# Kernel optimization log

Hardware: AMD Instinct MI355X
Metric: run time of the kernel (lower is better)

Reference implementation:

```python
import math
import jax, jax.numpy as jnp
import numpy as np

N_HEAD = 16
N_EMBD = 1024
HEAD_DIM = N_EMBD // N_HEAD  # 64
SHARED = 16
PRIV = HEAD_DIM - SHARED     # 48
B, T = 4, 2048
STD = 0.02


def setup_inputs() -> dict:
    key = jax.random.key(0)
    ks = jax.random.split(key, 6)
    x = jax.random.normal(ks[0], (B, T, N_EMBD), dtype=jnp.float32)
    # Linear params stored as (in, out); bias zeros per _reset_parameters
    W_share = jax.random.normal(ks[1], (N_EMBD, SHARED), dtype=jnp.float32) * STD
    Wq = jax.random.normal(ks[2], (N_EMBD, N_HEAD * PRIV), dtype=jnp.float32) * STD
    Wk = jax.random.normal(ks[3], (N_EMBD, N_HEAD * PRIV), dtype=jnp.float32) * STD
    Wv = jax.random.normal(ks[4], (N_EMBD, N_EMBD), dtype=jnp.float32) * STD
    Wo = jax.random.normal(ks[5], (N_EMBD, N_EMBD), dtype=jnp.float32) * STD
    return {
        'hidden_states': x,
        'W_share': W_share, 'b_share': jnp.zeros((SHARED,), jnp.float32),
        'Wq': Wq, 'bq': jnp.zeros((N_HEAD * PRIV,), jnp.float32),
        'Wk': Wk, 'bk': jnp.zeros((N_HEAD * PRIV,), jnp.float32),
        'Wv': Wv, 'bv': jnp.zeros((N_EMBD,), jnp.float32),
        'Wo': Wo, 'bo': jnp.zeros((N_EMBD,), jnp.float32),
    }


def reference(hidden_states, W_share, b_share, Wq, bq, Wk, bk, Wv, bv, Wo, bo):
    x = hidden_states
    Bt, Tt, C = x.shape
    # shared projection, broadcast across heads: (B,T,s) -> (B,H,T,s)
    share = x @ W_share + b_share
    share_h = jnp.broadcast_to(share[:, None, :, :], (Bt, N_HEAD, Tt, SHARED))
    # private q/k: (B,T,H*p) -> (B,H,T,p)
    q_priv = (x @ Wq + bq).reshape(Bt, Tt, N_HEAD, PRIV).transpose(0, 2, 1, 3)
    k_priv = (x @ Wk + bk).reshape(Bt, Tt, N_HEAD, PRIV).transpose(0, 2, 1, 3)
    q = jnp.concatenate([share_h, q_priv], axis=-1)  # (B,H,T,head_dim)
    k = jnp.concatenate([share_h, k_priv], axis=-1)
    v = (x @ Wv + bv).reshape(Bt, Tt, N_HEAD, HEAD_DIM).transpose(0, 2, 1, 3)
    scale = 1.0 / math.sqrt(HEAD_DIM)
    att = jnp.einsum('bhqd,bhkd->bhqk', q, k) * scale
    causal = jnp.tril(jnp.ones((Tt, Tt), dtype=bool))
    att = jnp.where(causal[None, None, :, :], att, -jnp.inf)
    att = jax.nn.softmax(att, axis=-1)
    y = jnp.einsum('bhqk,bhkd->bhqd', att, v)
    y = y.transpose(0, 2, 1, 3).reshape(Bt, Tt, C)
    y = y @ Wo + bo
    return y
```

## Files before the change

### kernel.cpp

```cpp
#include <hip/hip_runtime.h>
#include <hip/hip_bf16.h>

typedef unsigned short u16;
typedef short short8 __attribute__((ext_vector_type(8)));
typedef float f32x4 __attribute__((ext_vector_type(4)));
typedef float f32x16 __attribute__((ext_vector_type(16)));
typedef unsigned uint32x4 __attribute__((ext_vector_type(4)));

#define N_EMBD   1024
#define N_HEADS  16
#define HEAD_DIM 64
#define PRIV     48
#define SEQ_T    2048
#define BATCH    4
#define M_ROWS   (BATCH*SEQ_T)
#define PNS      2816
#define NTILES   (SEQ_T/64)
#define NT_K     16

#if __has_builtin(__builtin_amdgcn_exp2f)
#define EXP2(x) __builtin_amdgcn_exp2f(x)
#else
#define EXP2(x) exp2f(x)
#endif

#if __has_builtin(__builtin_amdgcn_global_load_lds)
#define HAVE_GLL 1
#else
#define HAVE_GLL 0
#endif

#if __has_builtin(__builtin_amdgcn_permlane32_swap)
#define HAVE_PLSWAP 1
typedef unsigned uint2v __attribute__((ext_vector_type(2)));
#else
#define HAVE_PLSWAP 0
#endif

__device__ __forceinline__ u16 f2bf(float f) {
  __hip_bfloat16 h = __float2bfloat16(f);
  return *reinterpret_cast<u16*>(&h);
}
__device__ __forceinline__ float bf2f(u16 s) {
  __hip_bfloat16 h;
  *reinterpret_cast<u16*>(&h) = s;
  return __bfloat162float(h);
}
__device__ __forceinline__ float loadv(const void* p, size_t i, int isf32) {
  return isf32 ? ((const float*)p)[i] : bf2f(((const u16*)p)[i]);
}
__device__ __forceinline__ u16 truncbf(float f) {
  unsigned u = __builtin_bit_cast(unsigned, f);
  return (u16)(u >> 16);
}
#if HAVE_GLL
__device__ __forceinline__ void gload_lds16(const u16* g, u16* l) {
  __builtin_amdgcn_global_load_lds(
      (const __attribute__((address_space(1))) void*)g,
      (__attribute__((address_space(3))) void*)l, 16, 0, 0);
}
#endif

__global__ __launch_bounds__(256) void detect_kernel(const u16* __restrict__ x,
                                                     int* __restrict__ flag) {
  __shared__ int cnt;
  if (threadIdx.x == 0) cnt = 0;
  __syncthreads();
  u16 v = x[2 * threadIdx.x];
  int e = (v >> 7) & 0xFF;
  int junk = (e >= 0xC0 || (e != 0 && e <= 0x30)) ? 1 : 0;
  if (junk) atomicAdd(&cnt, 1);
  __syncthreads();
  if (threadIdx.x == 0) *flag = (cnt > 16) ? 1 : 0;
}

__global__ __launch_bounds__(256) void pack_t_kernel(
    const void* __restrict__ Wsh, const void* __restrict__ Wq,
    const void* __restrict__ Wk,  const void* __restrict__ Wv,
    const void* __restrict__ Wo,
    const void* __restrict__ bsh, const void* __restrict__ bq,
    const void* __restrict__ bk,  const void* __restrict__ bv,
    const void* __restrict__ bo,
    u16* __restrict__ Wcat, u16* __restrict__ Woc,
    u16* __restrict__ bcat, u16* __restrict__ boc,
    const int* __restrict__ flagp)
{
  const int f = *flagp;
  if (blockIdx.z == 5) {
    const int flat = blockIdx.y * 16 + blockIdx.x;
    const int padN = (PNS - 2576) * 1024;
    for (int i = flat * 256 + threadIdx.x; i < padN; i += 256 * 256)
      Wcat[(size_t)2576 * 1024 + i] = 0;
    if (flat == 0) {
      for (int c = threadIdx.x; c < PNS; c += 256) {
        float v = 0.f;
        if (c < 16)        v = loadv(bsh, c, f);
        else if (c < 784)  v = loadv(bq, c - 16, f);
        else if (c < 1552) v = loadv(bk, c - 784, f);
        else if (c < 2576) v = loadv(bv, c - 1552, f);
        bcat[c] = f2bf(v);
      }
    } else if (flat == 1) {
      for (int c = threadIdx.x; c < N_EMBD; c += 256)
        boc[c] = f2bf(loadv(bo, c, f));
    }
    return;
  }
  const void* src; u16* dst; int N, rowOff;
  switch (blockIdx.z) {
    case 0: src = Wsh; dst = Wcat; N = 16;   rowOff = 0;    break;
    case 1: src = Wq;  dst = Wcat; N = 768;  rowOff = 16;   break;
    case 2: src = Wk;  dst = Wcat; N = 768;  rowOff = 784;  break;
    case 3: src = Wv;  dst = Wcat; N = 1024; rowOff = 1552; break;
    default:src = Wo;  dst = Woc;  N = 1024; rowOff = 0;    break;
  }
  const int n0 = blockIdx.x * 64;
  if (n0 >= N) return;
  const int k0 = blockIdx.y * 64;
  __shared__ u16 t[64][65];
  const int tx = threadIdx.x & 63, ty = threadIdx.x >> 6;
#pragma unroll
  for (int rr = 0; rr < 16; rr++) {
    int k = k0 + ty * 16 + rr;
    int n = n0 + tx;
    float v = (n < N) ? loadv(src, (size_t)k * N + n, f) : 0.f;
    t[ty * 16 + rr][tx] = f2bf(v);
  }
  __syncthreads();
#pragma unroll
  for (int rr = 0; rr < 16; rr++) {
    int n = ty * 16 + rr;
    if (n0 + n < N)
      dst[(size_t)(rowOff + n0 + n) * 1024 + k0 + tx] = t[tx][n];
  }
}

__global__ __launch_bounds__(256) void xbf_kernel(const void* __restrict__ x,
                                                  u16* __restrict__ Xb,
                                                  const int* __restrict__ flagp) {
  const int f = *flagp;
  const size_t i = (size_t)blockIdx.x * 256 + threadIdx.x;
  if (f) {
    const float4* p = (const float4*)x;
    float4 a = p[i * 2], b = p[i * 2 + 1];
    u16 t[8] = {f2bf(a.x), f2bf(a.y), f2bf(a.z), f2bf(a.w),
                f2bf(b.x), f2bf(b.y), f2bf(b.z), f2bf(b.w)};
    *(uint4*)&Xb[i * 8] = *(const uint4*)t;
  } else {
    *(uint4*)&Xb[i * 8] = ((const uint4*)x)[i];
  }
}

__global__ __launch_bounds__(512, 2) void gemm8p_kernel(
    const u16* __restrict__ A,
    const u16* __restrict__ Bt,
    const u16* __restrict__ bias,
    void* __restrict__ C, int ldc, int Mtiles,
    const int* __restrict__ flagp, int c_dyn)
{
  __shared__ __align__(16) u16 smem[73728];
  u16* const As = smem;
  u16* const Bs = smem + 3 * 8192;

  const bool cf32 = (c_dyn != 0) && (*flagp != 0);

  const int tid  = threadIdx.x;
  const int lane = tid & 63;
  const int w    = tid >> 6;
  const int quad = lane >> 4, l16 = lane & 15;
  const int wm   = w >> 2, wn = w & 3;

  const int nwg = gridDim.x;
  const int wg  = (blockIdx.x & 7) * (nwg >> 3) + (blockIdx.x >> 3);
  const int mb  = wg % Mtiles, nb = wg / Mtiles;
  const int m0  = mb * 128, n0 = nb * 256;

  int ldsA[2]; size_t glA[2];
  int ldsB[2][2]; size_t glB[2][2];
#pragma unroll
  for (int rd = 0; rd < 2; rd++) {
    int j = tid + rd * 512, rp = j >> 3, s = j & 7;
    int cl = (s ^ (rp & 7)) * 8;
    ldsA[rd] = rp * 64 + s * 8;
    glA[rd]  = (size_t)(m0 + rp) * 1024 + cl;
#pragma unroll
    for (int nh = 0; nh < 2; nh++) {
      int cc = (rp & 31) + nh * 32 + (rp >> 5) * 64;
      ldsB[nh][rd] = cc * 64 + s * 8;
      glB[nh][rd]  = (size_t)(n0 + cc) * 1024 + cl;
    }
  }

#if HAVE_GLL
#define G8(g, l) gload_lds16((g), (l))
#else
#define G8(g, l) (*(uint4*)(l) = *(const uint4*)(g))
#endif
#define STG_A(t, bf)                                                       \
  if ((t) < NT_K) {                                                        \
    _Pragma("unroll") for (int rd = 0; rd < 2; rd++)                       \
      G8(A + glA[rd] + (t) * 64, As + (bf) * 8192 + ldsA[rd]);             \
  }
#define STG_B(nh, t, bf)                                                   \
  if ((t) < NT_K) {                                                        \
    _Pragma("unroll") for (int rd = 0; rd < 2; rd++)                       \
      G8(Bt + glB[nh][rd] + (t) * 64, Bs + (bf) * 16384 + ldsB[nh][rd]);   \
  }

  const int ck0  = ((quad)     ^ (l16 & 7)) * 8;
  const int ck1  = ((4 + quad) ^ (l16 & 7)) * 8;
  const int arow = (wm * 64 + l16) * 64;
  const int brow = (wn * 64 + l16) * 64;

  f32x4 acc[4][4];
#pragma unroll
  for (int i = 0; i < 4; i++)
#pragma unroll
    for (int j = 0; j < 4; j++) acc[i][j] = (f32x4){0.f, 0.f, 0.f, 0.f};

  short8 af[4][2], bA[2][2], bB[2][2];

#define READ_A(cur)                                                        \
  { const u16* pa = As + (cur) * 8192 + arow;                              \
    _Pragma("unroll") for (int m = 0; m < 4; m++) {                        \
      af[m][0] = *(const short8*)(pa + m * 1024 + ck0);                    \
      af[m][1] = *(const short8*)(pa + m * 1024 + ck1); } }
#define READ_B(dst, nh, cur)                                               \
  { const u16* pb = Bs + (cur) * 16384 + brow + (nh) * 2048;               \
    _Pragma("unroll") for (int n = 0; n < 2; n++) {                        \
      dst[n][0] = *(const short8*)(pb + n * 1024 + ck0);                   \
      dst[n][1] = *(const short8*)(pb + n * 1024 + ck1); } }
#define MM16(bfr, nh)                                                      \
  __builtin_amdgcn_s_setprio(1);                                           \
  _Pragma("unroll") for (int m = 0; m < 4; m++)                            \
    _Pragma("unroll") for (int n = 0; n < 2; n++) {                        \
      acc[m][(nh)*2+n] = __builtin_amdgcn_mfma_f32_16x16x32_bf16(          \
          af[m][0], bfr[n][0], acc[m][(nh)*2+n], 0, 0, 0);                 \
      acc[m][(nh)*2+n] = __builtin_amdgcn_mfma_f32_16x16x32_bf16(          \
          af[m][1], bfr[n][1], acc[m][(nh)*2+n], 0, 0, 0); }               \
  __builtin_amdgcn_s_setprio(0);
#define BARR { __builtin_amdgcn_s_barrier(); __builtin_amdgcn_sched_barrier(0); }

  STG_A(0, 0); STG_B(1, 0, 0); STG_B(0, 0, 0);
  STG_A(1, 1); STG_B(1, 1, 1); STG_B(0, 1, 1);
  asm volatile("s_waitcnt vmcnt(6)");
  BARR;

#pragma unroll
  for (int kt = 0; kt < NT_K; kt++) {
    const int cur = kt % 3;
    const int stb = (kt + 2) % 3;
    READ_A(cur); READ_B(bA, 0, cur);
    STG_A(kt + 2, stb); STG_B(1, kt + 2, stb);
    BARR;
    MM16(bA, 0);
    BARR;
    READ_B(bB, 1, cur);
    STG_B(0, kt + 2, stb);
    BARR;
    MM16(bB, 1);
    if (kt < NT_K - 2)       { asm volatile("s_waitcnt vmcnt(6)"); }
    else if (kt == NT_K - 2) { asm volatile("s_waitcnt vmcnt(0)"); }
    BARR;
  }
#undef STG_A
#undef STG_B
#undef READ_A
#undef READ_B
#undef MM16
#undef BARR
#undef G8

  float bvv[4];
#pragma unroll
  for (int ni = 0; ni < 4; ni++)
    bvv[ni] = bf2f(bias[n0 + wn * 64 + ni * 16 + l16]);

  if (!cf32) {
    u16* cs = smem + w * 4096;
#pragma unroll
    for (int m = 0; m < 4; m++)
#pragma unroll
      for (int ni = 0; ni < 4; ni++)
#pragma unroll
        for (int r = 0; r < 4; r++) {
          int row = m * 16 + quad * 4 + r;
          int ch  = ((ni * 2 + (l16 >> 3)) ^ (row & 7)) * 8 + (l16 & 7);
          cs[row * 64 + ch] = f2bf(acc[m][ni][r] + bvv[ni]);
        }
    u16* Cb = (u16*)C;
#pragma unroll
    for (int i = 0; i < 8; i++) {
      int ch = lane + i * 64;
      int rr = ch >> 3, cc = ch & 7;
      short8 v = *(const short8*)(cs + rr * 64 + ((cc ^ (rr & 7)) * 8));
      *(short8*)&Cb[(size_t)(m0 + wm * 64 + rr) * ldc + n0 + wn * 64 + cc * 8] = v;
    }
  } else {
    float* cf = (float*)(void*)smem + w * 2048;
#pragma unroll
    for (int pass = 0; pass < 2; pass++) {
#pragma unroll
      for (int m2 = 0; m2 < 2; m2++)
#pragma unroll
        for (int ni = 0; ni < 4; ni++)
#pragma unroll
          for (int r = 0; r < 4; r++) {
            int row = m2 * 16 + quad * 4 + r;
            int ch  = ((ni * 4 + (l16 >> 2)) ^ (row & 15)) * 4 + (l16 & 3);
            cf[row * 64 + ch] = acc[pass * 2 + m2][ni][r] + bvv[ni];
          }
      float* Cf = (float*)C;
#pragma unroll
      for (int i = 0; i < 8; i++) {
        int ch = lane + i * 64;
        int rr = ch >> 4, cc = ch & 15;
        f32x4 v = *(const f32x4*)(cf + rr * 64 + ((cc ^ (rr & 15)) * 4));
        *(f32x4*)&Cf[(size_t)(m0 + wm * 64 + pass * 32 + rr) * ldc +
                     n0 + wn * 64 + cc * 4] = v;
      }
    }
  }
}

__global__ __launch_bounds__(256) void vt_kernel(const u16* __restrict__ P,
                                                 u16* __restrict__ Vt)
{
  const int tt = blockIdx.x * 64;
  const int bh = blockIdx.y;
  const int b = bh >> 4, h = bh & 15;
  const int vcol = 1552 + h * HEAD_DIM;
  __shared__ u16 t[64][65];
  const int tx = threadIdx.x & 63, ty = threadIdx.x >> 6;
#pragma unroll
  for (int rr = 0; rr < 16; rr++) {
    int r = ty * 16 + rr;
    t[r][tx] = P[((size_t)b * SEQ_T + tt + r) * PNS + vcol + tx];
  }
  __syncthreads();
#pragma unroll
  for (int rr = 0; rr < 16; rr++) {
    int d = ty * 16 + rr;
    Vt[((size_t)bh * 64 + d) * SEQ_T + tt + tx] = t[tx][d];
  }
}

__global__ __launch_bounds__(256, 3) void attn_kernel(
    const u16* __restrict__ P, const u16* __restrict__ Vt,
    u16* __restrict__ Y)
{
  const int bh  = blockIdx.x;
  const int b   = bh >> 4, h = bh & 15;
  const int j   = blockIdx.y;
  const int qtA = 2 * j, qtB = 2 * j + 1;
  const int tid = threadIdx.x;
  const int w   = tid >> 6;
  const int lane = tid & 63;
  const int l32 = lane & 31, hi = lane >> 5;
  const size_t rowb = (size_t)b * SEQ_T;
  const int qcol = 16 + h * PRIV;
  const int kcol = 784 + h * PRIV;

  __shared__ __align__(16) u16 Ks[3][64 * 64];
  __shared__ __align__(16) u16 Vs[3][64 * 64];

  const float csc = 0.18033688011112042f;
  const int iA = qtA * 64 + w * 16, iB = qtB * 64 + w * 16;
  const int gi = (l32 < 16) ? (iA + l32) : (iB + l32 - 16);
  const u16* qptr = P + (rowb + gi) * PNS;

  short8 qb[4];
  qb[0] = *(const short8*)&qptr[8 * hi];
#pragma unroll
  for (int c = 1; c < 4; c++)
    qb[c] = *(const short8*)&qptr[qcol + 16 * c + 8 * hi - 16];
#pragma unroll
  for (int c = 0; c < 4; c++)
#pragma unroll
    for (int e = 0; e < 8; e++)
      qb[c][e] = (short)f2bf(bf2f((u16)qb[c][e]) * csc);

  short8 ones;
#pragma unroll
  for (int e = 0; e < 8; e++) ones[e] = (short)0x3F80;

  const int nkt = qtB + 1;

#if HAVE_GLL
#define GLOADA(g, l) gload_lds16((g), (l))
#else
#define GLOADA(g, l) (*(uint4*)(l) = *(const uint4*)(g))
#endif
#define STAGE_KV(t, bb)                                                        \
  {                                                                            \
    const int kk0 = (t) * 64;                                                  \
    _Pragma("unroll") for (int i2 = 0; i2 < 2; i2++) {                         \
      int c   = tid + i2 * 256;                                                \
      int row = c >> 3;                                                        \
      int dg  = ((c & 7) ^ (row & 7)) * 8;                                     \
      int col = (dg < 16) ? dg : (kcol + dg - 16);                             \
      GLOADA(&P[(rowb + kk0 + row) * PNS + col], &Ks[bb][c * 8]);              \
      GLOADA(&Vt[((size_t)bh * 64 + row) * SEQ_T + kk0 + dg], &Vs[bb][c * 8]); \
    }                                                                          \
  }

  f32x16 accy[2], accl;
#pragma unroll
  for (int r = 0; r < 16; r++) { accy[0][r] = 0.f; accy[1][r] = 0.f; accl[r] = 0.f; }

  const float ninf = -__builtin_inff();

  STAGE_KV(0, 0);
  STAGE_KV(1, 1);
  asm volatile("s_waitcnt vmcnt(4)" ::: "memory");
  __builtin_amdgcn_sched_barrier(0);
  __builtin_amdgcn_s_barrier();

  for (int kt = 0; kt < nkt; kt++) {
    const int cur = kt % 3;
    const int k0  = kt * 64;
    if (kt + 2 < nkt) STAGE_KV(kt + 2, (kt + 2) % 3);

#pragma unroll
    for (int kk = 0; kk < 2; kk++) {
      f32x16 s;
#pragma unroll
      for (int r = 0; r < 16; r++) s[r] = 0.f;
      const int krow = kk * 32 + l32;
      __builtin_amdgcn_s_setprio(1);
#pragma unroll
      for (int c = 0; c < 4; c++) {
        short8 ka = *(const short8*)&Ks[cur][krow * 64 + (((2 * c + hi) ^ (krow & 7)) * 8)];
        s = __builtin_amdgcn_mfma_f32_32x32x16_bf16(ka, qb[c], s, 0, 0, 0);
      }
      __builtin_amdgcn_s_setprio(0);

      if (kt == qtA || kt == qtB) {
#pragma unroll
        for (int r = 0; r < 16; r++) {
          int gj = k0 + kk * 32 + (r & 3) + 8 * (r >> 2) + 4 * hi;
          if (gj > gi) s[r] = ninf;
        }
      }
      if (kt > qtA) {
#pragma unroll
        for (int r = 0; r < 16; r++)
          if (l32 < 16) s[r] = ninf;
      }

      float px[16];
#pragma unroll
      for (int r = 0; r < 16; r++) px[r] = EXP2(s[r]);

#pragma unroll
      for (int kc = 0; kc < 2; kc++) {
        unsigned g0, g1, g2, g3;
        asm("v_cvt_pk_bf16_f32 %0, %1, %2" : "=v"(g0) : "v"(px[8*kc+0]), "v"(px[8*kc+1]));
        asm("v_cvt_pk_bf16_f32 %0, %1, %2" : "=v"(g1) : "v"(px[8*kc+2]), "v"(px[8*kc+3]));
        asm("v_cvt_pk_bf16_f32 %0, %1, %2" : "=v"(g2) : "v"(px[8*kc+4]), "v"(px[8*kc+5]));
        asm("v_cvt_pk_bf16_f32 %0, %1, %2" : "=v"(g3) : "v"(px[8*kc+6]), "v"(px[8*kc+7]));
#if HAVE_PLSWAP
        uint2v r02 = __builtin_amdgcn_permlane32_swap(g0, g2, false, false);
        uint2v r13 = __builtin_amdgcn_permlane32_swap(g1, g3, false, false);
        uint32x4 pv = {r02.x, r13.x, r02.y, r13.y};
#else
        unsigned a0 = g0, b0 = g2, a1 = g1, b1 = g3;
        asm("v_permlane32_swap_b32 %0, %1" : "+v"(a0), "+v"(b0));
        asm("v_permlane32_swap_b32 %0, %1" : "+v"(a1), "+v"(b1));
        uint32x4 pv = {a0, a1, b0, b1};
#endif
        short8 pa = __builtin_bit_cast(short8, pv);

        __builtin_amdgcn_s_setprio(1);
        accl = __builtin_amdgcn_mfma_f32_32x32x16_bf16(pa, ones, accl, 0, 0, 0);
#pragma unroll
        for (int dt = 0; dt < 2; dt++) {
          int vrow = dt * 32 + l32;
          short8 vbf = *(const short8*)&Vs[cur][vrow * 64 + (((4*kk + 2*kc + hi) ^ (vrow & 7)) * 8)];
          accy[dt] = __builtin_amdgcn_mfma_f32_32x32x16_bf16(pa, vbf, accy[dt], 0, 0, 0);
        }
        __builtin_amdgcn_s_setprio(0);
      }
    }

    if (kt + 3 < nkt) {
      asm volatile("s_waitcnt vmcnt(4)" ::: "memory");
      __builtin_amdgcn_sched_barrier(0);
      __builtin_amdgcn_s_barrier();
    } else if (kt + 2 == nkt) {
      asm volatile("s_waitcnt vmcnt(0)" ::: "memory");
      __builtin_amdgcn_sched_barrier(0);
      __builtin_amdgcn_s_barrier();
    } else if (kt + 3 == nkt) {
      asm volatile("s_waitcnt vmcnt(4)" ::: "memory");
      __builtin_amdgcn_sched_barrier(0);
      __builtin_amdgcn_s_barrier();
    }
  }
#undef STAGE_KV
#undef GLOADA

  float inv[16];
#pragma unroll
  for (int r = 0; r < 16; r++) inv[r] = 1.0f / accl[r];
#pragma unroll
  for (int r = 0; r < 16; r++) {
    int q = (r & 3) + 8 * (r >> 2) + 4 * hi;
    int grow = (r < 8) ? (iA + q) : (iB + q - 16);
    size_t base = (rowb + grow) * N_EMBD + h * HEAD_DIM + l32;
    Y[base]      = f2bf(accy[0][r] * inv[r]);
    Y[base + 32] = f2bf(accy[1][r] * inv[r]);
  }
}

extern "C" void kernel_launch(void* const* d_in, const int* in_sizes, int n_in,
                              void* d_out, int out_size, void* d_ws, size_t ws_size,
                              hipStream_t stream) {
  (void)in_sizes; (void)n_in; (void)out_size; (void)ws_size;
  const void* x   = d_in[0];
  const void* Wsh = d_in[1];
  const void* bsh = d_in[2];
  const void* Wq  = d_in[3];
  const void* bq  = d_in[4];
  const void* Wk  = d_in[5];
  const void* bk  = d_in[6];
  const void* Wv  = d_in[7];
  const void* bv  = d_in[8];
  const void* Wo  = d_in[9];
  const void* bo  = d_in[10];

  char* wsb = (char*)d_ws;
  int* flag = (int*)wsb;
  u16* ws16 = (u16*)(wsb + 64);
  u16* Wcat = ws16;
  u16* bcat = Wcat + (size_t)PNS * N_EMBD;
  u16* Woc  = bcat + PNS;
  u16* boc  = Woc + (size_t)N_EMBD * N_EMBD;
  u16* Pb   = boc + N_EMBD;
  u16* Yb   = Pb + (size_t)M_ROWS * PNS;
  u16* Vtb  = Yb + (size_t)M_ROWS * N_EMBD;
  u16* Xb   = Yb;

  detect_kernel<<<dim3(1), dim3(256), 0, stream>>>((const u16*)x, flag);
  pack_t_kernel<<<dim3(16, 16, 6), dim3(256), 0, stream>>>(
      Wsh, Wq, Wk, Wv, Wo, bsh, bq, bk, bv, bo, Wcat, Woc, bcat, boc, flag);
  xbf_kernel<<<dim3(M_ROWS * N_EMBD / (256 * 8)), dim3(256), 0, stream>>>(
      x, Xb, flag);
  gemm8p_kernel<<<dim3(64 * (PNS / 256)), dim3(512), 0, stream>>>(
      Xb, Wcat, bcat, Pb, PNS, 64, flag, 0);
  vt_kernel<<<dim3(SEQ_T / 64, BATCH * N_HEADS), dim3(256), 0, stream>>>(
      Pb, Vtb);
  attn_kernel<<<dim3(BATCH * N_HEADS, NTILES / 2), dim3(256), 0, stream>>>(
      Pb, Vtb, Yb);
  gemm8p_kernel<<<dim3(64 * (N_EMBD / 256)), dim3(512), 0, stream>>>(
      Yb, Woc, boc, d_out, N_EMBD, 64, flag, 1);
}
```

Baseline: 275.3 us.

## Fuse V transpose into QKV GEMM epilogue and reverse attention tile order

Realigns the packed Q/K/V column offsets so V starts on a 64-column boundary, which lets the QKV GEMM epilogue write V directly in transposed per-head layout. This removes the separate vt_kernel launch and its extra global read and write of V. The attention grid is also reversed so the heaviest causal tiles launch first, improving load balance. In exchange the weight matrix gains padding rows, and the GEMM takes an extra barrier plus a branchy epilogue.

```diff
diff --git a/kernel.cpp b/kernel.cpp
--- a/kernel.cpp
+++ b/kernel.cpp
@@ -15,6 +15,9 @@
 #define BATCH    4
 #define M_ROWS   (BATCH*SEQ_T)
 #define PNS      2816
+#define QOFF     64
+#define KOFF     832
+#define VOFF     1600
 #define NTILES   (SEQ_T/64)
 #define NT_K     16
 
@@ -88,16 +91,20 @@
   const int f = *flagp;
   if (blockIdx.z == 5) {
     const int flat = blockIdx.y * 16 + blockIdx.x;
-    const int padN = (PNS - 2576) * 1024;
-    for (int i = flat * 256 + threadIdx.x; i < padN; i += 256 * 256)
-      Wcat[(size_t)2576 * 1024 + i] = 0;
+    const int padRows = 48 + 192;
+    for (int i = flat * 256 + threadIdx.x; i < padRows * 1024; i += 256 * 256) {
+      int r = i >> 10, c2 = i & 1023;
+      int row = (r < 48) ? (16 + r) : (2624 + (r - 48));
+      Wcat[(size_t)row * 1024 + c2] = 0;
+    }
     if (flat == 0) {
       for (int c = threadIdx.x; c < PNS; c += 256) {
         float v = 0.f;
-        if (c < 16)        v = loadv(bsh, c, f);
-        else if (c < 784)  v = loadv(bq, c - 16, f);
-        else if (c < 1552) v = loadv(bk, c - 784, f);
-        else if (c < 2576) v = loadv(bv, c - 1552, f);
+        if (c < 16)         v = loadv(bsh, c, f);
+        else if (c < QOFF)  v = 0.f;
+        else if (c < KOFF)  v = loadv(bq, c - QOFF, f);
+        else if (c < VOFF)  v = loadv(bk, c - KOFF, f);
+        else if (c < 2624)  v = loadv(bv, c - VOFF, f);
         bcat[c] = f2bf(v);
       }
     } else if (flat == 1) {
@@ -109,9 +116,9 @@
   const void* src; u16* dst; int N, rowOff;
   switch (blockIdx.z) {
     case 0: src = Wsh; dst = Wcat; N = 16;   rowOff = 0;    break;
-    case 1: src = Wq;  dst = Wcat; N = 768;  rowOff = 16;   break;
-    case 2: src = Wk;  dst = Wcat; N = 768;  rowOff = 784;  break;
-    case 3: src = Wv;  dst = Wcat; N = 1024; rowOff = 1552; break;
+    case 1: src = Wq;  dst = Wcat; N = 768;  rowOff = QOFF; break;
+    case 2: src = Wk;  dst = Wcat; N = 768;  rowOff = KOFF; break;
+    case 3: src = Wv;  dst = Wcat; N = 1024; rowOff = VOFF; break;
     default:src = Wo;  dst = Woc;  N = 1024; rowOff = 0;    break;
   }
   const int n0 = blockIdx.x * 64;
@@ -156,7 +163,8 @@
     const u16* __restrict__ Bt,
     const u16* __restrict__ bias,
     void* __restrict__ C, int ldc, int Mtiles,
-    const int* __restrict__ flagp, int c_dyn)
+    const int* __restrict__ flagp, int c_dyn,
+    u16* __restrict__ VtOut, int vt_en)
 {
   __shared__ __align__(16) u16 smem[73728];
   u16* const As = smem;
@@ -271,12 +279,39 @@
 #undef BARR
 #undef G8
 
+  __syncthreads();
+
   float bvv[4];
 #pragma unroll
   for (int ni = 0; ni < 4; ni++)
     bvv[ni] = bf2f(bias[n0 + wn * 64 + ni * 16 + l16]);
 
-  if (!cf32) {
+  const int ncol0 = n0 + wn * 64;
+  if (vt_en && ncol0 >= VOFF && ncol0 < VOFF + 1024) {
+    u16* cs = smem + w * 4096;
+#pragma unroll
+    for (int m = 0; m < 4; m++)
+#pragma unroll
+      for (int ni = 0; ni < 4; ni++)
+#pragma unroll
+        for (int r = 0; r < 4; r++) {
+          int d  = ni * 16 + l16;
+          int tc = m * 2 + (quad >> 1);
+          int te = (quad & 1) * 4 + r;
+          cs[d * 64 + ((tc ^ (d & 7)) * 8) + te] = f2bf(acc[m][ni][r] + bvv[ni]);
+        }
+    const int bb = (m0 + wm * 64) >> 11;
+    const int t0 = (m0 + wm * 64) & 2047;
+    const int hh = (ncol0 - VOFF) >> 6;
+    __builtin_amdgcn_s_barrier();
+#pragma unroll
+    for (int i = 0; i < 8; i++) {
+      int ch = lane + i * 64;
+      int rr = ch >> 3, cc = ch & 7;
+      short8 v = *(const short8*)(cs + rr * 64 + ((cc ^ (rr & 7)) * 8));
+      *(short8*)&VtOut[((size_t)(bb * 16 + hh) * 64 + rr) * SEQ_T + t0 + cc * 8] = v;
+    }
+  } else if (!cf32) {
     u16* cs = smem + w * 4096;
 #pragma unroll
     for (int m = 0; m < 4; m++)
@@ -323,43 +358,21 @@
   }
 }
 
-__global__ __launch_bounds__(256) void vt_kernel(const u16* __restrict__ P,
-                                                 u16* __restrict__ Vt)
-{
-  const int tt = blockIdx.x * 64;
-  const int bh = blockIdx.y;
-  const int b = bh >> 4, h = bh & 15;
-  const int vcol = 1552 + h * HEAD_DIM;
-  __shared__ u16 t[64][65];
-  const int tx = threadIdx.x & 63, ty = threadIdx.x >> 6;
-#pragma unroll
-  for (int rr = 0; rr < 16; rr++) {
-    int r = ty * 16 + rr;
-    t[r][tx] = P[((size_t)b * SEQ_T + tt + r) * PNS + vcol + tx];
-  }
-  __syncthreads();
-#pragma unroll
-  for (int rr = 0; rr < 16; rr++) {
-    int d = ty * 16 + rr;
-    Vt[((size_t)bh * 64 + d) * SEQ_T + tt + tx] = t[tx][d];
-  }
-}
-
 __global__ __launch_bounds__(256, 3) void attn_kernel(
     const u16* __restrict__ P, const u16* __restrict__ Vt,
     u16* __restrict__ Y)
 {
   const int bh  = blockIdx.x;
   const int b   = bh >> 4, h = bh & 15;
-  const int j   = blockIdx.y;
+  const int j   = 15 - blockIdx.y;
   const int qtA = 2 * j, qtB = 2 * j + 1;
   const int tid = threadIdx.x;
   const int w   = tid >> 6;
   const int lane = tid & 63;
   const int l32 = lane & 31, hi = lane >> 5;
   const size_t rowb = (size_t)b * SEQ_T;
-  const int qcol = 16 + h * PRIV;
-  const int kcol = 784 + h * PRIV;
+  const int qcol = QOFF + h * PRIV;
+  const int kcol = KOFF + h * PRIV;
 
   __shared__ __align__(16) u16 Ks[3][64 * 64];
   __shared__ __align__(16) u16 Vs[3][64 * 64];
@@ -547,11 +560,9 @@
   xbf_kernel<<<dim3(M_ROWS * N_EMBD / (256 * 8)), dim3(256), 0, stream>>>(
       x, Xb, flag);
   gemm8p_kernel<<<dim3(64 * (PNS / 256)), dim3(512), 0, stream>>>(
-      Xb, Wcat, bcat, Pb, PNS, 64, flag, 0);
-  vt_kernel<<<dim3(SEQ_T / 64, BATCH * N_HEADS), dim3(256), 0, stream>>>(
-      Pb, Vtb);
+      Xb, Wcat, bcat, Pb, PNS, 64, flag, 0, Vtb, 1);
   attn_kernel<<<dim3(BATCH * N_HEADS, NTILES / 2), dim3(256), 0, stream>>>(
       Pb, Vtb, Yb);
   gemm8p_kernel<<<dim3(64 * (N_EMBD / 256)), dim3(512), 0, stream>>>(
-      Yb, Woc, boc, d_out, N_EMBD, 64, flag, 1);
-}
+      Yb, Woc, boc, d_out, N_EMBD, 64, flag, 1, nullptr, 0);
+}
```

Result: faster. 261.0 us (-5.2%).
